# Performance work log

Hardware: AMD Instinct MI355X
Metric: run time of the kernel (lower is better)

The kernel has to match this reference:

```python
import jax, jax.numpy as jnp
import numpy as np

R = 0.15          # ball-query radius (module init arg r)
K = 32            # _MAX_NEIGHBOURS
B, N = 8, 4096


def _ball_query(pos, r, k):
    """Dense ball query. pos: [B,N,3] -> neighbor idx [B,N,K], sorted by distance.
    Slots with fewer than k in-radius neighbors are filled with the query's own
    index (self is always the first neighbor at distance 0), so their
    contribution to (f_i - f_j)^2 is exactly 0 -- matching torch-points-kernels'
    fill-with-first-neighbor behaviour."""
    d2 = jnp.sum((pos[:, :, None, :] - pos[:, None, :, :]) ** 2, axis=-1)  # [B,N,N]
    masked = jnp.where(d2 <= r * r, d2, jnp.inf)
    neg_vals, idx = jax.lax.top_k(-masked, k)          # ascending distance
    valid = neg_vals > -jnp.inf
    self_idx = jnp.arange(pos.shape[1])[None, :, None]
    return jnp.where(valid, idx, self_idx)             # [B,N,K]


def setup_inputs() -> dict:
    key = jax.random.key(0)
    k1, k2 = jax.random.split(key)
    pos = jax.random.uniform(k1, (B, N, 3), dtype=jnp.float32)
    f = jax.random.normal(k2, (B, N), dtype=jnp.float32)
    return {"pos": pos, "f": f}


def reference(pos, f):
    # neighbor indices are non-differentiable (torch gathers with long indices)
    nei_idx = jax.lax.stop_gradient(_ball_query(pos, R, K))      # [B,N,K]
    f_nei = jax.vmap(lambda fb, ib: fb[ib])(f, nei_idx)          # [B,N,K]
    variances = jnp.sum((f[:, :, None] - f_nei) ** 2, axis=-1)   # [B,N]
    return 0.5 * jnp.mean(variances)
```

## Files before the change

### kernel.cpp

```cpp
#include <hip/hip_runtime.h>


#define BQ_K 32
#define CAP 128
#define WPB 4
#define G 6
#define NC (G * G * G)
#define CAPC 832
#define QMAX 64

__device__ __forceinline__ int cell_coord(float x) {
    int c = (int)(x * (float)G);
    return c < 0 ? 0 : (c > G - 1 ? G - 1 : c);
}

__global__ __launch_bounds__(256) void dl_fused(
    const float* __restrict__ pos, const float* __restrict__ f,
    float* __restrict__ out, int N, float r2, float scale)
{
    __shared__ float4 s_cand[CAPC + 64];
    __shared__ float2 s_sel[WPB][CAP];
    __shared__ int    s_q[QMAX];
    __shared__ int    s_ncand, s_nq;
    __shared__ float  s_wsum[WPB];

    const int bc = blockIdx.x;
    const int b  = bc / NC;
    const int c  = bc - b * NC;
    const int cx = c % G, cy = (c / G) % G, cz = c / (G * G);

    const int lane = threadIdx.x & 63;
    const int wave = threadIdx.x >> 6;

    if (threadIdx.x == 0) { s_ncand = 0; s_nq = 0; }
    __syncthreads();

    const float* posb = pos + (size_t)b * N * 3;
    const float* fb   = f   + (size_t)b * N;

    const int per = N >> 2;
    const int wbeg = wave * per;
    for (int j0 = 0; j0 < per; j0 += 64) {
        const int j = wbeg + j0 + lane;
        const float x = posb[(size_t)j * 3 + 0];
        const float y = posb[(size_t)j * 3 + 1];
        const float z = posb[(size_t)j * 3 + 2];
        const float fj = fb[j];
        const int ccx = cell_coord(x), ccy = cell_coord(y), ccz = cell_coord(z);
        const bool in = (unsigned)(ccx - cx + 1) <= 2u &&
                        (unsigned)(ccy - cy + 1) <= 2u &&
                        (unsigned)(ccz - cz + 1) <= 2u;
        const unsigned long long m = __ballot(in);
        const int nh = __popcll(m);
        int base = 0;
        if (lane == 0 && nh) base = atomicAdd(&s_ncand, nh);
        base = __shfl(base, 0, 64);
        if (in) {
            const int off = base + __popcll(m & ((1ULL << lane) - 1ULL));
            if (off < CAPC) {
                s_cand[off] = make_float4(x, y, z, fj);
                if (ccx == cx && ccy == cy && ccz == cz) {
                    const int qs = atomicAdd(&s_nq, 1);
                    if (qs < QMAX) s_q[qs] = off;
                }
            }
        }
    }
    __syncthreads();

    const int ncand = s_ncand < CAPC ? s_ncand : CAPC;
    const int nq    = s_nq < QMAX ? s_nq : QMAX;
    const int ncp   = (ncand + 63) & ~63;
    for (int t = ncand + threadIdx.x; t < ncp; t += 256)
        s_cand[t] = make_float4(1e30f, 1e30f, 1e30f, 0.0f);
    __syncthreads();

    float2* sel = s_sel[wave];
    float wsum = 0.0f;

    for (int qi = wave; qi < nq; qi += WPB) {
        const float4 qp = s_cand[s_q[qi]];
        const float qx = qp.x, qy = qp.y, qz = qp.z, fi = qp.w;

        int cin = 0;
        for (int basej = 0; basej < ncp; basej += 64) {
            const float4 cd = s_cand[basej + lane];
            const float dx = cd.x - qx, dy = cd.y - qy, dz = cd.z - qz;
            const float d2 = fmaf(dx, dx, fmaf(dy, dy, dz * dz));
            const bool inb = (d2 <= r2);
            const unsigned long long mm = __ballot(inb);
            const int off = cin + __popcll(mm & ((1ULL << lane) - 1ULL));
            if (inb && off < CAP) {
                const float fd = fi - cd.w;
                sel[off] = make_float2(d2, fd * fd);
            }
            cin += __popcll(mm);
        }
        const int M = cin < CAP ? cin : CAP;

        const float2 e0 = (lane < M) ? sel[lane]
                                     : make_float2(1e30f, 0.0f);
        const float2 e1 = (64 + lane < M) ? sel[64 + lane]
                                          : make_float2(1e30f, 0.0f);

        if (M <= BQ_K) {
            wsum += e0.y + e1.y;
        } else {
            float lo = 0.0f, hi = r2 * 1.000001f;
            #pragma unroll
            for (int it = 0; it < 26; ++it) {
                const float mid = 0.5f * (lo + hi);
                const int cnt = __popcll(__ballot(e0.x < mid)) +
                                __popcll(__ballot(e1.x < mid));
                if (cnt >= BQ_K) hi = mid; else lo = mid;
            }
            if (e0.x < hi) wsum += e0.y;
            if (e1.x < hi) wsum += e1.y;
        }
    }

    for (int o = 32; o > 0; o >>= 1) wsum += __shfl_down(wsum, o, 64);
    if (lane == 0) s_wsum[wave] = wsum;
    __syncthreads();
    if (threadIdx.x == 0) {
        const float bs = s_wsum[0] + s_wsum[1] + s_wsum[2] + s_wsum[3];
        atomicAdd(out, bs * scale);
    }
}

extern "C" void kernel_launch(void* const* d_in, const int* in_sizes, int n_in,
                              void* d_out, int out_size, void* d_ws, size_t ws_size,
                              hipStream_t stream) {
    const float* pos = (const float*)d_in[0];
    const float* f   = (const float*)d_in[1];
    float* out = (float*)d_out;

    const int N = 4096;
    const int B = in_sizes[1] / N;
    const float r2 = 0.15f * 0.15f;
    const float scale = 0.5f / (float)((long long)B * N);

    hipMemsetAsync(out, 0, sizeof(float), stream);
    dl_fused<<<B * NC, 256, 0, stream>>>(pos, f, out, N, r2, scale);
}
```

Measured before the change: 93.11 us.

## Process two queries per wave, prefetch candidates, shorten threshold bisection

Each wave now handles two query points per pass over the candidate list, so each shared-memory candidate load feeds two distance tests. Global position loads and shared candidate loads are software-prefetched one iteration ahead. The padding fill and its extra barrier are replaced by a validity mask. The top-k threshold bisection drops from 26 to 14 iterations, which coarsens the radius threshold and risks picking the wrong neighbour when distances nearly tie, at the cost of more registers and double the selection buffers.

```diff
diff --git a/kernel.cpp b/kernel.cpp
--- a/kernel.cpp
+++ b/kernel.cpp
@@ -8,18 +8,36 @@
 #define NC (G * G * G)
 #define CAPC 832
 #define QMAX 64
+#define NPTS 4096
 
 __device__ __forceinline__ int cell_coord(float x) {
     int c = (int)(x * (float)G);
     return c < 0 ? 0 : (c > G - 1 ? G - 1 : c);
 }
 
+__device__ __forceinline__ float select_sum(float2 e0, float2 e1, int M,
+                                            float r2) {
+    if (M <= BQ_K) return e0.y + e1.y;
+    float lo = 0.0f, hi = r2 * 1.000001f;
+    #pragma unroll
+    for (int it = 0; it < 14; ++it) {
+        const float mid = 0.5f * (lo + hi);
+        const int cnt = __popcll(__ballot(e0.x < mid)) +
+                        __popcll(__ballot(e1.x < mid));
+        if (cnt >= BQ_K) hi = mid; else lo = mid;
+    }
+    float s = 0.0f;
+    if (e0.x < hi) s = e0.y;
+    if (e1.x < hi) s += e1.y;
+    return s;
+}
+
 __global__ __launch_bounds__(256) void dl_fused(
     const float* __restrict__ pos, const float* __restrict__ f,
-    float* __restrict__ out, int N, float r2, float scale)
+    float* __restrict__ out, float r2, float scale)
 {
-    __shared__ float4 s_cand[CAPC + 64];
-    __shared__ float2 s_sel[WPB][CAP];
+    __shared__ float4 s_cand[CAPC];
+    __shared__ float2 s_sel[WPB][2][CAP];
     __shared__ int    s_q[QMAX];
     __shared__ int    s_ncand, s_nq;
     __shared__ float  s_wsum[WPB];
@@ -31,22 +49,32 @@
 
     const int lane = threadIdx.x & 63;
     const int wave = threadIdx.x >> 6;
+    const unsigned long long lmask = (1ULL << lane) - 1ULL;
 
     if (threadIdx.x == 0) { s_ncand = 0; s_nq = 0; }
     __syncthreads();
 
-    const float* posb = pos + (size_t)b * N * 3;
-    const float* fb   = f   + (size_t)b * N;
+    const float* posb = pos + (size_t)b * NPTS * 3;
+    const float* fb   = f   + (size_t)b * NPTS;
 
-    const int per = N >> 2;
+    constexpr int per = NPTS / WPB;
     const int wbeg = wave * per;
+    int jp = wbeg + lane;
+    float x  = posb[3 * jp + 0];
+    float y  = posb[3 * jp + 1];
+    float z  = posb[3 * jp + 2];
+    float fj = fb[jp];
     for (int j0 = 0; j0 < per; j0 += 64) {
-        const int j = wbeg + j0 + lane;
-        const float x = posb[(size_t)j * 3 + 0];
-        const float y = posb[(size_t)j * 3 + 1];
-        const float z = posb[(size_t)j * 3 + 2];
-        const float fj = fb[j];
-        const int ccx = cell_coord(x), ccy = cell_coord(y), ccz = cell_coord(z);
+        const float xx = x, yy = y, zz = z, ff = fj;
+        if (j0 + 64 < per) {
+            const int jn = wbeg + j0 + 64 + lane;
+            x  = posb[3 * jn + 0];
+            y  = posb[3 * jn + 1];
+            z  = posb[3 * jn + 2];
+            fj = fb[jn];
+        }
+        const int ccx = cell_coord(xx), ccy = cell_coord(yy),
+                  ccz = cell_coord(zz);
         const bool in = (unsigned)(ccx - cx + 1) <= 2u &&
                         (unsigned)(ccy - cy + 1) <= 2u &&
                         (unsigned)(ccz - cz + 1) <= 2u;
@@ -56,9 +84,9 @@
         if (lane == 0 && nh) base = atomicAdd(&s_ncand, nh);
         base = __shfl(base, 0, 64);
         if (in) {
-            const int off = base + __popcll(m & ((1ULL << lane) - 1ULL));
+            const int off = base + __popcll(m & lmask);
             if (off < CAPC) {
-                s_cand[off] = make_float4(x, y, z, fj);
+                s_cand[off] = make_float4(xx, yy, zz, ff);
                 if (ccx == cx && ccy == cy && ccz == cz) {
                     const int qs = atomicAdd(&s_nq, 1);
                     if (qs < QMAX) s_q[qs] = off;
@@ -70,52 +98,69 @@
 
     const int ncand = s_ncand < CAPC ? s_ncand : CAPC;
     const int nq    = s_nq < QMAX ? s_nq : QMAX;
-    const int ncp   = (ncand + 63) & ~63;
-    for (int t = ncand + threadIdx.x; t < ncp; t += 256)
-        s_cand[t] = make_float4(1e30f, 1e30f, 1e30f, 0.0f);
-    __syncthreads();
+    const int ncB   = (ncand + 63) & ~63;
 
-    float2* sel = s_sel[wave];
+    float2* sel0 = s_sel[wave][0];
+    float2* sel1 = s_sel[wave][1];
     float wsum = 0.0f;
 
-    for (int qi = wave; qi < nq; qi += WPB) {
-        const float4 qp = s_cand[s_q[qi]];
-        const float qx = qp.x, qy = qp.y, qz = qp.z, fi = qp.w;
+    for (int qi = wave * 2; qi < nq; qi += WPB * 2) {
+        const float4 qp0 = s_cand[s_q[qi]];
+        const bool  has1 = (qi + 1) < nq;
+        const float4 qp1 = has1 ? s_cand[s_q[qi + 1]]
+                                : make_float4(1e30f, 1e30f, 1e30f, 0.0f);
 
-        int cin = 0;
-        for (int basej = 0; basej < ncp; basej += 64) {
-            const float4 cd = s_cand[basej + lane];
-            const float dx = cd.x - qx, dy = cd.y - qy, dz = cd.z - qz;
-            const float d2 = fmaf(dx, dx, fmaf(dy, dy, dz * dz));
-            const bool inb = (d2 <= r2);
-            const unsigned long long mm = __ballot(inb);
-            const int off = cin + __popcll(mm & ((1ULL << lane) - 1ULL));
-            if (inb && off < CAP) {
-                const float fd = fi - cd.w;
-                sel[off] = make_float2(d2, fd * fd);
+        int cin0 = 0, cin1 = 0;
+        float4 nxt = s_cand[lane];
+        for (int basej = 0; basej < ncB; basej += 64) {
+            const float4 cd = nxt;
+            if (basej + 64 < ncB) nxt = s_cand[basej + 64 + lane];
+            const bool valid = (basej + lane) < ncand;
+
+            const float dx0 = cd.x - qp0.x, dy0 = cd.y - qp0.y,
+                        dz0 = cd.z - qp0.z;
+            const float d20 = fmaf(dx0, dx0, fmaf(dy0, dy0, dz0 * dz0));
+            const float dx1 = cd.x - qp1.x, dy1 = cd.y - qp1.y,
+                        dz1 = cd.z - qp1.z;
+            const float d21 = fmaf(dx1, dx1, fmaf(dy1, dy1, dz1 * dz1));
+
+            const bool in0 = valid && (d20 <= r2);
+            const bool in1 = valid && (d21 <= r2);
+            const unsigned long long m0 = __ballot(in0);
+            const unsigned long long m1 = __ballot(in1);
+            if (in0) {
+                const int off = cin0 + __popcll(m0 & lmask);
+                if (off < CAP) {
+                    const float fd = qp0.w - cd.w;
+                    sel0[off] = make_float2(d20, fd * fd);
+                }
             }
-            cin += __popcll(mm);
+            if (in1) {
+                const int off = cin1 + __popcll(m1 & lmask);
+                if (off < CAP) {
+                    const float fd = qp1.w - cd.w;
+                    sel1[off] = make_float2(d21, fd * fd);
+                }
+            }
+            cin0 += __popcll(m0);
+            cin1 += __popcll(m1);
         }
-        const int M = cin < CAP ? cin : CAP;
+        const int M0 = cin0 < CAP ? cin0 : CAP;
+        const int M1 = cin1 < CAP ? cin1 : CAP;
 
-        const float2 e0 = (lane < M) ? sel[lane]
-                                     : make_float2(1e30f, 0.0f);
-        const float2 e1 = (64 + lane < M) ? sel[64 + lane]
+        {
+            const float2 a0 = (lane < M0) ? sel0[lane]
                                           : make_float2(1e30f, 0.0f);
-
-        if (M <= BQ_K) {
-            wsum += e0.y + e1.y;
-        } else {
-            float lo = 0.0f, hi = r2 * 1.000001f;
-            #pragma unroll
-            for (int it = 0; it < 26; ++it) {
-                const float mid = 0.5f * (lo + hi);
-                const int cnt = __popcll(__ballot(e0.x < mid)) +
-                                __popcll(__ballot(e1.x < mid));
-                if (cnt >= BQ_K) hi = mid; else lo = mid;
-            }
-            if (e0.x < hi) wsum += e0.y;
-            if (e1.x < hi) wsum += e1.y;
+            const float2 a1 = (64 + lane < M0) ? sel0[64 + lane]
+                                               : make_float2(1e30f, 0.0f);
+            wsum += select_sum(a0, a1, M0, r2);
+        }
+        {
+            const float2 b0 = (lane < M1) ? sel1[lane]
+                                          : make_float2(1e30f, 0.0f);
+            const float2 b1 = (64 + lane < M1) ? sel1[64 + lane]
+                                               : make_float2(1e30f, 0.0f);
+            wsum += select_sum(b0, b1, M1, r2);
         }
     }
 
@@ -135,11 +180,10 @@
     const float* f   = (const float*)d_in[1];
     float* out = (float*)d_out;
 
-    const int N = 4096;
-    const int B = in_sizes[1] / N;
+    const int B = in_sizes[1] / NPTS;
     const float r2 = 0.15f * 0.15f;
-    const float scale = 0.5f / (float)((long long)B * N);
+    const float scale = 0.5f / (float)((long long)B * NPTS);
 
     hipMemsetAsync(out, 0, sizeof(float), stream);
-    dl_fused<<<B * NC, 256, 0, stream>>>(pos, f, out, N, r2, scale);
+    dl_fused<<<B * NC, 256, 0, stream>>>(pos, f, out, r2, scale);
 }
```

Result: slower. 95.62 us (+2.7%).

## Prune candidates by exact cell-box distance and shorten top-k bisection

Applied to the files above, without the earlier changes.

The candidate filter now keeps only points whose squared distance to the query cell's box is within r², instead of every point in the 3x3x3 cell neighbourhood. This shrinks the per-query candidate scan, so the candidate buffer is cut from 832 to 512 entries. The padding pass and its extra barrier are replaced by a validity mask, and the radius bisection drops from 26 to 14 iterations. Shortening the bisection risks tie or precision errors in the 32-nearest selection when distances are close. The smaller buffer risks overflow in dense regions, which would silently drop candidates.

```diff
diff --git a/kernel.cpp b/kernel.cpp
--- a/kernel.cpp
+++ b/kernel.cpp
@@ -6,19 +6,37 @@
 #define WPB 4
 #define G 6
 #define NC (G * G * G)
-#define CAPC 832
+#define CAPC 512
 #define QMAX 64
+#define NPTS 4096
 
 __device__ __forceinline__ int cell_coord(float x) {
     int c = (int)(x * (float)G);
     return c < 0 ? 0 : (c > G - 1 ? G - 1 : c);
 }
 
+__device__ __forceinline__ float select_sum(float2 e0, float2 e1, int M,
+                                            float r2) {
+    if (M <= BQ_K) return e0.y + e1.y;
+    float lo = 0.0f, hi = r2 * 1.000001f;
+    #pragma unroll
+    for (int it = 0; it < 14; ++it) {
+        const float mid = 0.5f * (lo + hi);
+        const int cnt = __popcll(__ballot(e0.x < mid)) +
+                        __popcll(__ballot(e1.x < mid));
+        if (cnt >= BQ_K) hi = mid; else lo = mid;
+    }
+    float s = 0.0f;
+    if (e0.x < hi) s = e0.y;
+    if (e1.x < hi) s += e1.y;
+    return s;
+}
+
 __global__ __launch_bounds__(256) void dl_fused(
     const float* __restrict__ pos, const float* __restrict__ f,
-    float* __restrict__ out, int N, float r2, float scale)
+    float* __restrict__ out, float r2, float scale)
 {
-    __shared__ float4 s_cand[CAPC + 64];
+    __shared__ float4 s_cand[CAPC];
     __shared__ float2 s_sel[WPB][CAP];
     __shared__ int    s_q[QMAX];
     __shared__ int    s_ncand, s_nq;
@@ -31,35 +49,42 @@
 
     const int lane = threadIdx.x & 63;
     const int wave = threadIdx.x >> 6;
+    const unsigned long long lmask = (1ULL << lane) - 1ULL;
 
     if (threadIdx.x == 0) { s_ncand = 0; s_nq = 0; }
     __syncthreads();
 
-    const float* posb = pos + (size_t)b * N * 3;
-    const float* fb   = f   + (size_t)b * N;
+    const float* posb = pos + (size_t)b * NPTS * 3;
+    const float* fb   = f   + (size_t)b * NPTS;
 
-    const int per = N >> 2;
+    const float lox = cx * (1.0f / G), hix = lox + (1.0f / G);
+    const float loy = cy * (1.0f / G), hiy = loy + (1.0f / G);
+    const float loz = cz * (1.0f / G), hiz = loz + (1.0f / G);
+
+    constexpr int per = NPTS / WPB;
     const int wbeg = wave * per;
     for (int j0 = 0; j0 < per; j0 += 64) {
         const int j = wbeg + j0 + lane;
-        const float x = posb[(size_t)j * 3 + 0];
-        const float y = posb[(size_t)j * 3 + 1];
-        const float z = posb[(size_t)j * 3 + 2];
+        const float x  = posb[3 * j + 0];
+        const float y  = posb[3 * j + 1];
+        const float z  = posb[3 * j + 2];
         const float fj = fb[j];
-        const int ccx = cell_coord(x), ccy = cell_coord(y), ccz = cell_coord(z);
-        const bool in = (unsigned)(ccx - cx + 1) <= 2u &&
-                        (unsigned)(ccy - cy + 1) <= 2u &&
-                        (unsigned)(ccz - cz + 1) <= 2u;
+        const float ddx = fmaxf(fmaxf(lox - x, x - hix), 0.0f);
+        const float ddy = fmaxf(fmaxf(loy - y, y - hiy), 0.0f);
+        const float ddz = fmaxf(fmaxf(loz - z, z - hiz), 0.0f);
+        const float d2c = fmaf(ddx, ddx, fmaf(ddy, ddy, ddz * ddz));
+        const bool in = (d2c <= r2);
         const unsigned long long m = __ballot(in);
         const int nh = __popcll(m);
         int base = 0;
         if (lane == 0 && nh) base = atomicAdd(&s_ncand, nh);
         base = __shfl(base, 0, 64);
         if (in) {
-            const int off = base + __popcll(m & ((1ULL << lane) - 1ULL));
+            const int off = base + __popcll(m & lmask);
             if (off < CAPC) {
                 s_cand[off] = make_float4(x, y, z, fj);
-                if (ccx == cx && ccy == cy && ccz == cz) {
+                if (cell_coord(x) == cx && cell_coord(y) == cy &&
+                    cell_coord(z) == cz) {
                     const int qs = atomicAdd(&s_nq, 1);
                     if (qs < QMAX) s_q[qs] = off;
                 }
@@ -70,10 +95,7 @@
 
     const int ncand = s_ncand < CAPC ? s_ncand : CAPC;
     const int nq    = s_nq < QMAX ? s_nq : QMAX;
-    const int ncp   = (ncand + 63) & ~63;
-    for (int t = ncand + threadIdx.x; t < ncp; t += 256)
-        s_cand[t] = make_float4(1e30f, 1e30f, 1e30f, 0.0f);
-    __syncthreads();
+    const int ncB   = (ncand + 63) & ~63;
 
     float2* sel = s_sel[wave];
     float wsum = 0.0f;
@@ -83,13 +105,14 @@
         const float qx = qp.x, qy = qp.y, qz = qp.z, fi = qp.w;
 
         int cin = 0;
-        for (int basej = 0; basej < ncp; basej += 64) {
+        for (int basej = 0; basej < ncB; basej += 64) {
             const float4 cd = s_cand[basej + lane];
+            const bool valid = (basej + lane) < ncand;
             const float dx = cd.x - qx, dy = cd.y - qy, dz = cd.z - qz;
             const float d2 = fmaf(dx, dx, fmaf(dy, dy, dz * dz));
-            const bool inb = (d2 <= r2);
+            const bool inb = valid && (d2 <= r2);
             const unsigned long long mm = __ballot(inb);
-            const int off = cin + __popcll(mm & ((1ULL << lane) - 1ULL));
+            const int off = cin + __popcll(mm & lmask);
             if (inb && off < CAP) {
                 const float fd = fi - cd.w;
                 sel[off] = make_float2(d2, fd * fd);
@@ -102,21 +125,7 @@
                                      : make_float2(1e30f, 0.0f);
         const float2 e1 = (64 + lane < M) ? sel[64 + lane]
                                           : make_float2(1e30f, 0.0f);
-
-        if (M <= BQ_K) {
-            wsum += e0.y + e1.y;
-        } else {
-            float lo = 0.0f, hi = r2 * 1.000001f;
-            #pragma unroll
-            for (int it = 0; it < 26; ++it) {
-                const float mid = 0.5f * (lo + hi);
-                const int cnt = __popcll(__ballot(e0.x < mid)) +
-                                __popcll(__ballot(e1.x < mid));
-                if (cnt >= BQ_K) hi = mid; else lo = mid;
-            }
-            if (e0.x < hi) wsum += e0.y;
-            if (e1.x < hi) wsum += e1.y;
-        }
+        wsum += select_sum(e0, e1, M, r2);
     }
 
     for (int o = 32; o > 0; o >>= 1) wsum += __shfl_down(wsum, o, 64);
@@ -135,11 +144,10 @@
     const float* f   = (const float*)d_in[1];
     float* out = (float*)d_out;
 
-    const int N = 4096;
-    const int B = in_sizes[1] / N;
+    const int B = in_sizes[1] / NPTS;
     const float r2 = 0.15f * 0.15f;
-    const float scale = 0.5f / (float)((long long)B * N);
+    const float scale = 0.5f / (float)((long long)B * NPTS);
 
     hipMemsetAsync(out, 0, sizeof(float), stream);
-    dl_fused<<<B * NC, 256, 0, stream>>>(pos, f, out, N, r2, scale);
+    dl_fused<<<B * NC, 256, 0, stream>>>(pos, f, out, r2, scale);
 }
```

Measured after the change: 89.15 us. 1.04x faster.
